# Kernel optimization log

Measured on AMD Instinct MI355X. Metric: run time of the kernel, lower is better.

The kernel has to match this reference:

```python
import jax, jax.numpy as jnp
import numpy as np

B = 2048        # batch
D_IN = 512      # input_dim
H = 768         # hidden_dim
A = 5001        # num_atoms
RULE_LEN = 4
N_DATA = 56000.0


def setup_inputs() -> dict:
    key = jax.random.key(0)
    ks = jax.random.split(key, 24)
    def w(k, shape, fan):
        return (jax.random.normal(k, shape, jnp.float32) / np.sqrt(fan)).astype(jnp.float32)
    return {
        'x': jax.random.normal(ks[0], (B, D_IN), jnp.float32),
        'x_mask': jax.random.randint(ks[1], (B, A), 0, 2, jnp.int32),
        # linear_base: Linear(512,768) ReLU Linear(768,768) ReLU Linear(768,768)
        'W1': w(ks[2], (H, D_IN), D_IN), 'b1': jnp.zeros((H,), jnp.float32),
        'W2': w(ks[3], (H, H), H),       'b2': jnp.zeros((H,), jnp.float32),
        'W3': w(ks[4], (H, H), H),       'b3': jnp.zeros((H,), jnp.float32),
        # single-layer GRU (input H, hidden H); gates ordered r,z,n as in torch
        'W_ih': w(ks[5], (3 * H, H), H), 'b_ih': jnp.zeros((3 * H,), jnp.float32),
        'W_hh': w(ks[6], (3 * H, H), H), 'b_hh': jnp.zeros((3 * H,), jnp.float32),
        # gru_head: Linear(H, num_atoms)
        'Wh': w(ks[7], (A, H), H), 'bh': jnp.zeros((A,), jnp.float32),
        # atom embedding table
        'ae_weight': jax.random.normal(ks[8], (A, H), jnp.float32) * 0.02,
        # stand-in consequent estimator heads (mu, coverage)
        'w_mu': w(ks[9], (H, 1), H),  'b_mu': jnp.zeros((1,), jnp.float32),
        'w_cov': w(ks[10], (H, 1), H), 'b_cov': jnp.zeros((1,), jnp.float32),
        'alpha': jnp.ones((1,), jnp.float32),
    }


def _gru_step(xt, h, W_ih, b_ih, W_hh, b_hh):
    gi = xt @ W_ih.T + b_ih
    gh = h @ W_hh.T + b_hh
    i_r, i_z, i_n = jnp.split(gi, 3, axis=-1)
    h_r, h_z, h_n = jnp.split(gh, 3, axis=-1)
    r = jax.nn.sigmoid(i_r + h_r)
    z = jax.nn.sigmoid(i_z + h_z)
    n = jnp.tanh(i_n + r * h_n)
    return (1.0 - z) * n + z * h


def reference(x, x_mask, W1, b1, W2, b2, W3, b3, W_ih, b_ih, W_hh, b_hh,
              Wh, bh, ae_weight, w_mu, b_mu, w_cov, b_cov, alpha):
    # base (dnn) encoder -> cls embedding [B, H]
    cls = jax.nn.relu(x @ W1.T + b1)
    cls = jax.nn.relu(cls @ W2.T + b2)
    cls = cls @ W3.T + b3

    ae_det = jax.lax.stop_gradient(ae_weight)  # ae.weight is always detached in the original
    mask = x_mask.astype(jnp.float32)
    h = jnp.zeros_like(cls)
    cur = cls
    probs = []
    idx = None
    gkey = jax.random.key(42)
    batch_idx = jnp.arange(cls.shape[0])

    for j in range(RULE_LEN):
        h = _gru_step(cur, h, W_ih, b_ih, W_hh, b_hh)  # dropout = identity (eval)
        logits = h @ Wh.T + bh  # [B, A]
        if j == 0:
            row_zero = jnp.sum(mask, axis=1) == 0.0
            mask = mask.at[:, 0].set(jnp.where(row_zero, 1.0, mask[:, 0]))
        else:
            mask = jnp.where((idx == 0)[:, None], 0.0, mask)
            mask = mask.at[:, 0].set(1.0)
        masked = jnp.where(mask > 0.0, logits, -jnp.inf)
        # gumbel-softmax, tau=1, hard=True (straight-through)
        u = jax.random.uniform(jax.random.fold_in(gkey, j), masked.shape,
                               jnp.float32, 1e-6, 1.0 - 1e-6)
        g = -jnp.log(-jnp.log(u))
        y_soft = jax.nn.softmax(masked + g, axis=1)
        idx = jnp.argmax(y_soft, axis=1)
        y_hard = jax.nn.one_hot(idx, A, dtype=y_soft.dtype)
        prob = y_hard + y_soft - jax.lax.stop_gradient(y_soft)
        probs.append(prob)
        # scatter zero at the selected atom so it can't repeat
        mask = mask.at[batch_idx, idx].set(0.0)
        cur = cls + prob @ ae_det  # [B, H]

    atom_prob = jnp.stack(probs, axis=1)  # [B, rule_len, A]
    atoms = jnp.einsum('bra,ad->brd', atom_prob, ae_det)  # [B, rule_len, H]

    # stand-in consequent estimator: (mu, coverage) from summed atoms
    a = jnp.sum(atoms, axis=1)
    mu = jax.nn.sigmoid(a @ w_mu + b_mu)[:, 0]
    coverage = jax.nn.sigmoid(a @ w_cov + b_cov)[:, 0]

    n = coverage * N_DATA
    inv = alpha[0] / n
    pp = (mu + inv) / (1.0 + 2.0 * inv)
    cp = jnp.stack([1.0 - pp, pp], axis=-1)  # [B, 2]
    out = jnp.log(cp)  # head=1 -> mean over heads is identity
    return (out, atom_prob, cp)
```

## Files before the change

### kernel.cpp

```cpp
#include <hip/hip_runtime.h>
#include <stdint.h>
#include <math.h>

#define B_    2048
#define DIN_  512
#define H_    768
#define G3_   2304
#define A_    5001
#define APAD_ 5120
#define RL_   4
#define NDATA_ 56000.0f

typedef _Float16 f16x8 __attribute__((ext_vector_type(8)));
typedef _Float16 f16x4 __attribute__((ext_vector_type(4)));
typedef float    f32x4 __attribute__((ext_vector_type(4)));

__host__ __device__ __forceinline__ void threefry2x32(
    uint32_t k0, uint32_t k1, uint32_t x0, uint32_t x1,
    uint32_t* o0, uint32_t* o1)
{
  const uint32_t ks2 = k0 ^ k1 ^ 0x1BD11BDAu;
#define TF_R(r) { x0 += x1; x1 = (x1 << (r)) | (x1 >> (32 - (r))); x1 ^= x0; }
  x0 += k0; x1 += k1;
  TF_R(13) TF_R(15) TF_R(26) TF_R(6)
  x0 += k1;  x1 += ks2 + 1u;
  TF_R(17) TF_R(29) TF_R(16) TF_R(24)
  x0 += ks2; x1 += k0 + 2u;
  TF_R(13) TF_R(15) TF_R(26) TF_R(6)
  x0 += k0;  x1 += k1 + 3u;
  TF_R(17) TF_R(29) TF_R(16) TF_R(24)
  x0 += k1;  x1 += ks2 + 4u;
  TF_R(13) TF_R(15) TF_R(26) TF_R(6)
  x0 += ks2; x1 += k0 + 5u;
#undef TF_R
  *o0 = x0; *o1 = x1;
}

__device__ __forceinline__ float gumbel_for(uint32_t k0, uint32_t k1, uint32_t n)
{
  uint32_t o0, o1;
  threefry2x32(k0, k1, 0u, n, &o0, &o1);
  const uint32_t bits = o0 ^ o1;
  const float f = __uint_as_float((bits >> 9) | 0x3f800000u);
  const float minv = 1e-6f;
  const float maxv = 1.0f - 1e-6f;
  const float span = maxv - minv;
  float u = __fmul_rn(f, span);
  u = __fadd_rn(u, minv);
  u = __fsub_rn(u, span);
  u = fmaxf(minv, u);
  return -logf(-logf(u));
}

struct HL { _Float16 h, l; };
__device__ __forceinline__ HL split64(float v)
{
  HL r;
  const float s = v * 64.f;
  r.h = (_Float16)s;
  r.l = (_Float16)(s - (float)r.h);
  return r;
}

__device__ __forceinline__ void gload16(const void* g, void* l)
{
  __builtin_amdgcn_global_load_lds(
      (const __attribute__((address_space(1))) void*)g,
      (__attribute__((address_space(3))) void*)l, 16, 0, 0);
}

struct PSJobs {
  const float* src[7];
  _Float16* hi[7];
  _Float16* lo[7];
  int R[7]; int K[7];
  int cum[8];
};

__global__ __launch_bounds__(256)
void presplit_all(PSJobs J)
{
  const int g = blockIdx.x * 256 + threadIdx.x;
  if (g >= J.cum[7]) return;
  int j = 0;
  while (g >= J.cum[j + 1]) ++j;
  const int i = g - J.cum[j];
  const int K = J.K[j];
  const int e = i * 4;
  const int row = e / K;
  float4 f = make_float4(0.f, 0.f, 0.f, 0.f);
  if (row < J.R[j]) f = *(const float4*)(J.src[j] + (size_t)row * K + (e - row * K));
  const HL s0 = split64(f.x), s1 = split64(f.y);
  const HL s2 = split64(f.z), s3 = split64(f.w);
  const f16x4 hv = {s0.h, s1.h, s2.h, s3.h};
  ((f16x4*)J.hi[j])[i] = hv;
  if (J.lo[j]) {
    const f16x4 lv = {s0.l, s1.l, s2.l, s3.l};
    ((f16x4*)J.lo[j])[i] = lv;
  }
}

__global__ __launch_bounds__(256)
void prep_k(const int* __restrict__ xmask, uint8_t* __restrict__ mask,
            const float* __restrict__ Wh, float* __restrict__ wmaxsq,
            const float* __restrict__ x, _Float16* __restrict__ xh,
            _Float16* __restrict__ xl)
{
  const int blk = blockIdx.x, tid = threadIdx.x;
  __shared__ float redf[256];
  __shared__ int   redi[256];
  if (blk < B_) {
    const int b = blk;
    int s = 0;
    for (int a = tid; a < A_; a += 256) {
      const int m = (xmask[(size_t)b * A_ + a] != 0) ? 1 : 0;
      mask[(size_t)b * A_ + a] = (uint8_t)m;
      s += m;
    }
    redi[tid] = s; __syncthreads();
    for (int t = 128; t > 0; t >>= 1) {
      if (tid < t) redi[tid] += redi[tid + t];
      __syncthreads();
    }
    if (tid == 0 && redi[0] == 0) mask[(size_t)b * A_] = 1;
  } else if (blk < B_ + A_) {
    const int a = blk - B_;
    float p = 0.f;
    for (int d = tid; d < H_; d += 256) {
      const float w = Wh[(size_t)a * H_ + d];
      p += w * w;
    }
    redf[tid] = p; __syncthreads();
    for (int t = 128; t > 0; t >>= 1) {
      if (tid < t) redf[tid] += redf[tid + t];
      __syncthreads();
    }
    if (tid == 0) atomicMax((int*)wmaxsq, __float_as_int(redf[0]));
  } else {
    const int i = (blk - B_ - A_) * 256 + tid;
    const int n4 = B_ * DIN_ / 4;
    if (i < n4) {
      const float4 f = ((const float4*)x)[i];
      const HL s0 = split64(f.x), s1 = split64(f.y);
      const HL s2 = split64(f.z), s3 = split64(f.w);
      const f16x4 hv = {s0.h, s1.h, s2.h, s3.h};
      const f16x4 lv = {s0.l, s1.l, s2.l, s3.l};
      ((f16x4*)xh)[i] = hv;
      ((f16x4*)xl)[i] = lv;
    }
  }
}

struct GJob {
  const _Float16 *Ah, *Al, *Bh, *Bl;
  const float* bias;
  float* C;
  _Float16 *Ch, *Cl;
  int M, K, ldc, n0, Nv;
  int npass, act, wsplit, gum;
};
struct GArgs { GJob j[2]; int sx; uint32_t k0, k1; };

__global__ __launch_bounds__(256)
void gemm2job(GArgs P)
{
  __shared__ _Float16 sA[2][128 * 32];
  __shared__ _Float16 sB[2][128 * 32];

  const int jid = (blockIdx.x < P.sx) ? 0 : 1;
  const GJob J = P.j[jid];
  const int bxx = blockIdx.x - (jid ? P.sx : 0);
  const int bm = blockIdx.y * 128;
  if (bm >= J.M) return;
  const int bn = J.n0 + bxx * 128;

  const int tid = threadIdx.x;
  const int lane = tid & 63, wave = tid >> 6;
  const int wx = wave & 1, wy = wave >> 1;
  const int q = lane >> 4, mr = lane & 15;
  const int K = J.K;
  const int np3 = (J.npass == 3);

  f32x4 acc[4][4];
#pragma unroll
  for (int i = 0; i < 4; ++i)
#pragma unroll
    for (int j = 0; j < 4; ++j) acc[i][j] = (f32x4)0.f;

  const int abase = (wy * 64 + mr) * 32 + q * 8;
  const int bbase = (wx * 64 + mr) * 32 + q * 8;

  if (np3) {
    auto stage = [&](int k0) {
#pragma unroll
      for (int t = 0; t < 2; ++t) {
        const int c = wave * 2 + t;
        const int row = c * 16 + (lane >> 2);
        const int kc = (lane & 3) * 8;
        const size_t ga = (size_t)(bm + row) * K + k0 + kc;
        const size_t gb = (size_t)(bn + row) * K + k0 + kc;
        gload16(J.Ah + ga, &sA[0][c * 512]);
        gload16(J.Bh + gb, &sB[0][c * 512]);
        gload16(J.Al + ga, &sA[1][c * 512]);
        gload16(J.Bl + gb, &sB[1][c * 512]);
      }
    };
    stage(0);
    const int T = K / 32;
    for (int t = 0; t < T; ++t) {
      __syncthreads();
      f16x8 ah[4], al[4], bhv[4], blv[4];
#pragma unroll
      for (int mi = 0; mi < 4; ++mi) {
        ah[mi]  = *(const f16x8*)&sA[0][abase + mi * 512];
        bhv[mi] = *(const f16x8*)&sB[0][bbase + mi * 512];
        al[mi]  = *(const f16x8*)&sA[1][abase + mi * 512];
        blv[mi] = *(const f16x8*)&sB[1][bbase + mi * 512];
      }
      __syncthreads();
      if (t + 1 < T) stage((t + 1) * 32);
#pragma unroll
      for (int ni = 0; ni < 4; ++ni)
#pragma unroll
        for (int mi = 0; mi < 4; ++mi) {
          acc[mi][ni] = __builtin_amdgcn_mfma_f32_16x16x32_f16(ah[mi], bhv[ni], acc[mi][ni], 0, 0, 0);
          acc[mi][ni] = __builtin_amdgcn_mfma_f32_16x16x32_f16(al[mi], bhv[ni], acc[mi][ni], 0, 0, 0);
          acc[mi][ni] = __builtin_amdgcn_mfma_f32_16x16x32_f16(ah[mi], blv[ni], acc[mi][ni], 0, 0, 0);
        }
    }
  } else {
    auto stage64 = [&](int k0) {
#pragma unroll
      for (int t = 0; t < 2; ++t) {
        const int c = wave * 2 + t;
        const int row = c * 16 + (lane >> 2);
        const int kc = (lane & 3) * 8;
        const size_t ga = (size_t)(bm + row) * K + k0 + kc;
        const size_t gb = (size_t)(bn + row) * K + k0 + kc;
        gload16(J.Ah + ga, &sA[0][c * 512]);
        gload16(J.Bh + gb, &sB[0][c * 512]);
        gload16(J.Ah + ga + 32, &sA[1][c * 512]);
        gload16(J.Bh + gb + 32, &sB[1][c * 512]);
      }
    };
    stage64(0);
    const int T2 = K / 64;
    for (int t = 0; t < T2; ++t) {
      __syncthreads();
      f16x8 a0[4], b0[4];
#pragma unroll
      for (int mi = 0; mi < 4; ++mi) {
        a0[mi] = *(const f16x8*)&sA[0][abase + mi * 512];
        b0[mi] = *(const f16x8*)&sB[0][bbase + mi * 512];
      }
#pragma unroll
      for (int ni = 0; ni < 4; ++ni)
#pragma unroll
        for (int mi = 0; mi < 4; ++mi)
          acc[mi][ni] = __builtin_amdgcn_mfma_f32_16x16x32_f16(a0[mi], b0[ni], acc[mi][ni], 0, 0, 0);
      f16x8 a1[4], b1[4];
#pragma unroll
      for (int mi = 0; mi < 4; ++mi) {
        a1[mi] = *(const f16x8*)&sA[1][abase + mi * 512];
        b1[mi] = *(const f16x8*)&sB[1][bbase + mi * 512];
      }
      __syncthreads();
      if (t + 1 < T2) stage64((t + 1) * 64);
#pragma unroll
      for (int ni = 0; ni < 4; ++ni)
#pragma unroll
        for (int mi = 0; mi < 4; ++mi)
          acc[mi][ni] = __builtin_amdgcn_mfma_f32_16x16x32_f16(a1[mi], b1[ni], acc[mi][ni], 0, 0, 0);
    }
  }

  const float sc = 1.f / 4096.f;
#pragma unroll
  for (int ni = 0; ni < 4; ++ni) {
    const int n = bn + wx * 64 + ni * 16 + mr;
    if (n >= J.Nv) continue;
    const float bv = J.bias ? J.bias[n] : 0.f;
#pragma unroll
    for (int mi = 0; mi < 4; ++mi) {
      const int m0 = bm + wy * 64 + mi * 16 + q * 4;
#pragma unroll
      for (int r = 0; r < 4; ++r) {
        const int m = m0 + r;
        float v = acc[mi][ni][r] * sc + bv;
        if (J.act) v = fmaxf(v, 0.f);
        if (J.gum) v += gumbel_for(P.k0, P.k1, (uint32_t)(m * J.ldc + n));
        const size_t off = (size_t)m * J.ldc + n;
        if (J.C) J.C[off] = v;
        if (J.wsplit) {
          const HL s = split64(v);
          J.Ch[off] = s.h;
          J.Cl[off] = s.l;
        }
      }
    }
  }
}

__global__ __launch_bounds__(256)
void gru_elem(const float* __restrict__ gi, const float* __restrict__ bhh,
              float* __restrict__ h, _Float16* __restrict__ hh_,
              _Float16* __restrict__ hl_)
{
  const int i = blockIdx.x * 256 + threadIdx.x;
  if (i >= B_ * H_) return;
  const int b = i / H_;
  const int d = i - b * H_;
  const float* gib = gi + (size_t)b * G3_;
  const float ir = gib[d], iz = gib[H_ + d], in_ = gib[2 * H_ + d];
  const float hr = bhh[d], hz = bhh[H_ + d], hn = bhh[2 * H_ + d];
  const float r = 1.f / (1.f + expf(-(ir + hr)));
  const float z = 1.f / (1.f + expf(-(iz + hz)));
  const float n = tanhf(in_ + r * hn);
  const float hv = (1.f - z) * n;
  h[i] = hv;
  const HL s = split64(hv);
  hh_[i] = s.h; hl_[i] = s.l;
}

__global__ __launch_bounds__(256)
void select_step(const float* __restrict__ v, uint8_t* __restrict__ mask,
                 int* __restrict__ idxs, const float* __restrict__ giCls,
                 const float* __restrict__ AeWih, float* __restrict__ atomp,
                 float* __restrict__ hbuf, const float* __restrict__ WhF,
                 const float* __restrict__ bh, const float* __restrict__ wmaxsq,
                 const float* __restrict__ gh, const float* __restrict__ bhh,
                 _Float16* __restrict__ hh_, _Float16* __restrict__ hl_,
                 uint32_t k0, uint32_t k1, int step)
{
  const int b = blockIdx.x, tid = threadIdx.x;
  uint8_t* mrow = mask + (size_t)b * A_;
  __shared__ float vsh[A_];
  __shared__ float hsh[H_];
  __shared__ float gish[G3_];
  __shared__ float sv[256];
  __shared__ int   si[256];
  __shared__ int   s_list[64];
  __shared__ int   s_n;
  __shared__ int   s_sel;

  float hp = 0.f;
  for (int d = tid; d < H_; d += 256) {
    const float t = hbuf[(size_t)b * H_ + d];
    hsh[d] = t; hp += t * t;
  }
  sv[tid] = hp; __syncthreads();
  for (int t = 128; t > 0; t >>= 1) {
    if (tid < t) sv[tid] += sv[tid + t];
    __syncthreads();
  }
  const float hn2 = sv[0];
  __syncthreads();

  if (step > 0) {
    const int prev = idxs[(step - 1) * B_ + b];
    if (prev == 0)
      for (int a = tid; a < A_; a += 256) mrow[a] = 0;
    __syncthreads();
    if (tid == 0) mrow[0] = 1;
  }
  if (tid == 0) s_n = 0;
  __syncthreads();

  const float* vrow = v + (size_t)b * A_;
  float bv = -INFINITY; int bi = A_;
  for (int a = tid; a < A_; a += 256) {
    const float val = mrow[a] ? vrow[a] : -INFINITY;
    vsh[a] = val;
    if (val > bv) { bv = val; bi = a; }
  }
  sv[tid] = bv; si[tid] = bi; __syncthreads();
  for (int t = 128; t > 0; t >>= 1) {
    if (tid < t) {
      const float v2 = sv[tid + t]; const int i2 = si[tid + t];
      if (v2 > sv[tid] || (v2 == sv[tid] && i2 < si[tid])) { sv[tid] = v2; si[tid] = i2; }
    }
    __syncthreads();
  }
  const float amax = sv[0];
  __syncthreads();

  const float delta = 2.0f * 0.0009765625f * sqrtf(hn2 * wmaxsq[0]);
  const float thr = amax - 2.f * delta;

  for (int a = tid; a < A_; a += 256)
    if (vsh[a] >= thr) {
      const int p = atomicAdd(&s_n, 1);
      if (p < 64) s_list[p] = a;
    }
  __syncthreads();
  const int nc = (s_n < 64) ? s_n : 64;

  const uint32_t nbase = (uint32_t)b * (uint32_t)A_;
  float best = -INFINITY; int bestA = A_;
  for (int c = 0; c < nc; ++c) {
    const int a = s_list[c];
    const float* wr = WhF + (size_t)a * H_;
    float p = 0.f;
    for (int d = tid; d < H_; d += 256) p += hsh[d] * wr[d];
    sv[tid] = p; __syncthreads();
    for (int t = 128; t > 0; t >>= 1) {
      if (tid < t) sv[tid] += sv[tid + t];
      __syncthreads();
    }
    if (tid == 0) {
      const float ev = sv[0] + bh[a] + gumbel_for(k0, k1, nbase + (uint32_t)a);
      if (ev > best || (ev == best && a < bestA)) { best = ev; bestA = a; }
    }
    __syncthreads();
  }
  if (tid == 0) {
    s_sel = bestA;
    mrow[bestA] = 0;
    idxs[step * B_ + b] = bestA;
    atomp[(size_t)b * (RL_ * A_) + (size_t)step * A_ + bestA] = 1.0f;
  }
  __syncthreads();

  if (step < RL_ - 1) {
    const int sel = s_sel;
    const float* ar = AeWih + (size_t)sel * G3_;
    const float* gr = giCls + (size_t)b * G3_;
    for (int d = tid; d < G3_; d += 256) gish[d] = gr[d] + ar[d];
    __syncthreads();
    const float* ghb = gh + (size_t)b * G3_;
    for (int d = tid; d < H_; d += 256) {
      const float r = 1.f / (1.f + expf(-(gish[d] + ghb[d])));
      const float z = 1.f / (1.f + expf(-(gish[H_ + d] + ghb[H_ + d])));
      const float n = tanhf(gish[2 * H_ + d] + r * ghb[2 * H_ + d]);
      const float hv = (1.f - z) * n + z * hsh[d];
      hbuf[(size_t)b * H_ + d] = hv;
      const HL s = split64(hv);
      hh_[(size_t)b * H_ + d] = s.h;
      hl_[(size_t)b * H_ + d] = s.l;
    }
  }
}

__global__ __launch_bounds__(256)
void head_k(const int* __restrict__ idxs, const float* __restrict__ ae,
            const float* __restrict__ w_mu, const float* __restrict__ b_mu,
            const float* __restrict__ w_cov, const float* __restrict__ b_cov,
            const float* __restrict__ alpha, float* __restrict__ outf)
{
  const int b = blockIdx.x, tid = threadIdx.x;
  const int i0 = idxs[0 * B_ + b], i1 = idxs[1 * B_ + b];
  const int i2 = idxs[2 * B_ + b], i3 = idxs[3 * B_ + b];
  const float* r0 = ae + (size_t)i0 * H_;
  const float* r1 = ae + (size_t)i1 * H_;
  const float* r2 = ae + (size_t)i2 * H_;
  const float* r3 = ae + (size_t)i3 * H_;
  float pmu = 0.f, pcv = 0.f;
  for (int d = tid; d < H_; d += 256) {
    const float a = r0[d] + r1[d] + r2[d] + r3[d];
    pmu += a * w_mu[d];
    pcv += a * w_cov[d];
  }
  __shared__ float smu[256], scv[256];
  smu[tid] = pmu; scv[tid] = pcv;
  __syncthreads();
  for (int s = 128; s > 0; s >>= 1) {
    if (tid < s) { smu[tid] += smu[tid + s]; scv[tid] += scv[tid + s]; }
    __syncthreads();
  }
  if (tid == 0) {
    const float mu = 1.f / (1.f + expf(-(smu[0] + b_mu[0])));
    const float cv = 1.f / (1.f + expf(-(scv[0] + b_cov[0])));
    const float n = cv * NDATA_;
    const float inv = alpha[0] / n;
    const float pp = (mu + inv) / (1.f + 2.f * inv);
    outf[2 * b + 0] = logf(1.f - pp);
    outf[2 * b + 1] = logf(pp);
    float* cp = outf + 2 * B_ + (size_t)B_ * RL_ * A_;
    cp[2 * b + 0] = 1.f - pp;
    cp[2 * b + 1] = pp;
  }
}

extern "C" void kernel_launch(void* const* d_in, const int* in_sizes, int n_in,
                              void* d_out, int out_size, void* d_ws, size_t ws_size,
                              hipStream_t stream)
{
  const float* x     = (const float*)d_in[0];
  const int*   xmask = (const int*)d_in[1];
  const float* W1 = (const float*)d_in[2];  const float* b1 = (const float*)d_in[3];
  const float* W2 = (const float*)d_in[4];  const float* b2 = (const float*)d_in[5];
  const float* W3 = (const float*)d_in[6];  const float* b3 = (const float*)d_in[7];
  const float* Wih = (const float*)d_in[8]; const float* bih = (const float*)d_in[9];
  const float* Whh = (const float*)d_in[10];const float* bhh = (const float*)d_in[11];
  const float* Wh = (const float*)d_in[12]; const float* bh = (const float*)d_in[13];
  const float* ae = (const float*)d_in[14];
  const float* w_mu = (const float*)d_in[15];  const float* b_mu = (const float*)d_in[16];
  const float* w_cov = (const float*)d_in[17]; const float* b_cov = (const float*)d_in[18];
  const float* alpha = (const float*)d_in[19];

  char* ws = (char*)d_ws;
  size_t off = 0;
  auto alloc = [&](size_t bytes) -> void* {
    void* p = ws + off;
    off += (bytes + 255) & ~(size_t)255;
    return p;
  };
  float* hbuf   = (float*)alloc((size_t)B_ * H_ * 4);
  float* giCls  = (float*)alloc((size_t)B_ * G3_ * 4);
  float* gh     = (float*)alloc((size_t)B_ * G3_ * 4);
  float* vbuf   = (float*)alloc((size_t)B_ * A_ * 4);
  float* AeWih  = (float*)alloc((size_t)APAD_ * G3_ * 4);
  uint8_t* mask = (uint8_t*)alloc((size_t)B_ * A_);
  int* idxs     = (int*)alloc((size_t)RL_ * B_ * 4);
  _Float16* hh_ = (_Float16*)alloc((size_t)B_ * H_ * 2);
  _Float16* hl_ = (_Float16*)alloc((size_t)B_ * H_ * 2);
  _Float16* clsh = (_Float16*)alloc((size_t)B_ * H_ * 2);
  _Float16* clsl = (_Float16*)alloc((size_t)B_ * H_ * 2);
  _Float16* xh  = (_Float16*)alloc((size_t)B_ * DIN_ * 2);
  _Float16* xl  = (_Float16*)alloc((size_t)B_ * DIN_ * 2);
  _Float16* t1h = (_Float16*)alloc((size_t)B_ * H_ * 2);
  _Float16* t1l = (_Float16*)alloc((size_t)B_ * H_ * 2);
  _Float16* t2h = (_Float16*)alloc((size_t)B_ * H_ * 2);
  _Float16* t2l = (_Float16*)alloc((size_t)B_ * H_ * 2);
  _Float16* w1h = (_Float16*)alloc((size_t)H_ * DIN_ * 2);
  _Float16* w1l = (_Float16*)alloc((size_t)H_ * DIN_ * 2);
  _Float16* w2h = (_Float16*)alloc((size_t)H_ * H_ * 2);
  _Float16* w2l = (_Float16*)alloc((size_t)H_ * H_ * 2);
  _Float16* w3h = (_Float16*)alloc((size_t)H_ * H_ * 2);
  _Float16* w3l = (_Float16*)alloc((size_t)H_ * H_ * 2);
  _Float16* wihh = (_Float16*)alloc((size_t)G3_ * H_ * 2);
  _Float16* wihl = (_Float16*)alloc((size_t)G3_ * H_ * 2);
  _Float16* whhh = (_Float16*)alloc((size_t)G3_ * H_ * 2);
  _Float16* whhl = (_Float16*)alloc((size_t)G3_ * H_ * 2);
  _Float16* whhi = (_Float16*)alloc((size_t)APAD_ * H_ * 2);
  _Float16* aeh  = (_Float16*)alloc((size_t)APAD_ * H_ * 2);
  _Float16* ael  = (_Float16*)alloc((size_t)APAD_ * H_ * 2);
  float* wmaxsq = (float*)alloc(4);

  float* outf  = (float*)d_out;
  float* atomp = outf + 2 * B_;

  (void)hipMemsetAsync(d_out, 0, (size_t)out_size * sizeof(float), stream);
  (void)hipMemsetAsync(wmaxsq, 0, 4, stream);

  PSJobs J;
  const float* srcs[7] = {W1, W2, W3, Wih, Whh, Wh, ae};
  _Float16* his[7] = {w1h, w2h, w3h, wihh, whhh, whhi, aeh};
  _Float16* los[7] = {w1l, w2l, w3l, wihl, whhl, nullptr, ael};
  const int Rs[7]    = {H_, H_, H_, G3_, G3_, A_, A_};
  const int Rpads[7] = {H_, H_, H_, G3_, G3_, APAD_, APAD_};
  const int Ks[7]    = {DIN_, H_, H_, H_, H_, H_, H_};
  J.cum[0] = 0;
  for (int j = 0; j < 7; ++j) {
    J.src[j] = srcs[j]; J.hi[j] = his[j]; J.lo[j] = los[j];
    J.R[j] = Rs[j]; J.K[j] = Ks[j];
    J.cum[j + 1] = J.cum[j] + Rpads[j] * Ks[j] / 4;
  }
  presplit_all<<<(J.cum[7] + 255) / 256, 256, 0, stream>>>(J);

  prep_k<<<B_ + A_ + (B_ * DIN_ / 4 + 255) / 256, 256, 0, stream>>>(
      xmask, mask, Wh, wmaxsq, x, xh, xl);

  auto mkjob = [](const _Float16* Ah, const _Float16* Al, const _Float16* Bh,
                  const _Float16* Bl, const float* bias, float* C,
                  _Float16* Ch, _Float16* Cl, int M, int K, int ldc,
                  int n0, int Nv, int npass, int act, int wsplit, int gum) {
    GJob g; g.Ah = Ah; g.Al = Al; g.Bh = Bh; g.Bl = Bl; g.bias = bias;
    g.C = C; g.Ch = Ch; g.Cl = Cl; g.M = M; g.K = K; g.ldc = ldc;
    g.n0 = n0; g.Nv = Nv; g.npass = npass; g.act = act; g.wsplit = wsplit;
    g.gum = gum;
    return g;
  };
  auto aejob = [&](int t0) {
    return mkjob(aeh, ael, wihh, wihl, nullptr, AeWih, nullptr, nullptr,
                 APAD_, H_, G3_, t0 * 128, G3_, 3, 0, 0, 0);
  };

  {
    GArgs P;
    P.j[0] = mkjob(xh, xl, w1h, w1l, b1, nullptr, t1h, t1l,
                   B_, DIN_, H_, 0, H_, 3, 1, 1, 0);
    P.j[1] = aejob(0);
    P.sx = H_ / 128; P.k0 = 0; P.k1 = 0;
    gemm2job<<<dim3(H_ / 128 + 5, APAD_ / 128), 256, 0, stream>>>(P);
  }
  {
    GArgs P;
    P.j[0] = mkjob(t1h, t1l, w2h, w2l, b2, nullptr, t2h, t2l,
                   B_, H_, H_, 0, H_, 3, 1, 1, 0);
    P.j[1] = aejob(5);
    P.sx = H_ / 128; P.k0 = 0; P.k1 = 0;
    gemm2job<<<dim3(H_ / 128 + 5, APAD_ / 128), 256, 0, stream>>>(P);
  }
  {
    GArgs P;
    P.j[0] = mkjob(t2h, t2l, w3h, w3l, b3, nullptr, clsh, clsl,
                   B_, H_, H_, 0, H_, 3, 0, 1, 0);
    P.j[1] = aejob(10);
    P.sx = H_ / 128; P.k0 = 0; P.k1 = 0;
    gemm2job<<<dim3(H_ / 128 + 4, APAD_ / 128), 256, 0, stream>>>(P);
  }
  {
    GArgs P;
    P.j[0] = mkjob(clsh, clsl, wihh, wihl, bih, giCls, nullptr, nullptr,
                   B_, H_, G3_, 0, G3_, 3, 0, 0, 0);
    P.j[1] = aejob(14);
    P.sx = G3_ / 128; P.k0 = 0; P.k1 = 0;
    gemm2job<<<dim3(G3_ / 128 + 4, APAD_ / 128), 256, 0, stream>>>(P);
  }

  uint32_t fk0[RL_], fk1[RL_];
  for (int j = 0; j < RL_; ++j)
    threefry2x32(0u, 42u, 0u, (uint32_t)j, &fk0[j], &fk1[j]);

  gru_elem<<<(B_ * H_ + 255) / 256, 256, 0, stream>>>(giCls, bhh, hbuf, hh_, hl_);

  for (int j = 0; j < RL_; ++j) {
    GArgs P;
    P.j[0] = mkjob(hh_, nullptr, whhi, nullptr, bh, vbuf, nullptr, nullptr,
                   B_, H_, A_, 0, A_, 1, 0, 0, 1);
    const int gx0 = APAD_ / 128;
    int gx = gx0;
    if (j < RL_ - 1) {
      P.j[1] = mkjob(hh_, hl_, whhh, whhl, bhh, gh, nullptr, nullptr,
                     B_, H_, G3_, 0, G3_, 3, 0, 0, 0);
      gx += G3_ / 128;
    } else {
      P.j[1] = P.j[0];
    }
    P.sx = gx0; P.k0 = fk0[j]; P.k1 = fk1[j];
    gemm2job<<<dim3(gx, B_ / 128), 256, 0, stream>>>(P);

    select_step<<<B_, 256, 0, stream>>>(vbuf, mask, idxs, giCls, AeWih, atomp,
                                        hbuf, Wh, bh, wmaxsq, gh, bhh, hh_, hl_,
                                        fk0[j], fk1[j], j);
  }

  head_k<<<B_, 256, 0, stream>>>(idxs, ae, w_mu, b_mu, w_cov, b_cov, alpha, outf);
}
```

Before: 1.043 ms.

## Fold W3 into W_ih to drop a GEMM stage and trim select_step shared memory

```diff
diff --git a/kernel.cpp b/kernel.cpp
--- a/kernel.cpp
+++ b/kernel.cpp
@@ -73,7 +73,7 @@
   const float* src[7];
   _Float16* hi[7];
   _Float16* lo[7];
-  int R[7]; int K[7];
+  int R[7]; int K[7]; int trans[7];
   int cum[8];
 };
 
@@ -88,8 +88,17 @@
   const int K = J.K[j];
   const int e = i * 4;
   const int row = e / K;
+  const int col = e - row * K;
   float4 f = make_float4(0.f, 0.f, 0.f, 0.f);
-  if (row < J.R[j]) f = *(const float4*)(J.src[j] + (size_t)row * K + (e - row * K));
+  if (J.trans[j]) {
+    const int R = J.R[j];
+    f.x = J.src[j][(size_t)(col + 0) * R + row];
+    f.y = J.src[j][(size_t)(col + 1) * R + row];
+    f.z = J.src[j][(size_t)(col + 2) * R + row];
+    f.w = J.src[j][(size_t)(col + 3) * R + row];
+  } else if (row < J.R[j]) {
+    f = *(const float4*)(J.src[j] + (size_t)row * K + col);
+  }
   const HL s0 = split64(f.x), s1 = split64(f.y);
   const HL s2 = split64(f.z), s3 = split64(f.w);
   const f16x4 hv = {s0.h, s1.h, s2.h, s3.h};
@@ -104,9 +113,12 @@
 void prep_k(const int* __restrict__ xmask, uint8_t* __restrict__ mask,
             const float* __restrict__ Wh, float* __restrict__ wmaxsq,
             const float* __restrict__ x, _Float16* __restrict__ xh,
-            _Float16* __restrict__ xl)
+            _Float16* __restrict__ xl, const float* __restrict__ Wih,
+            const float* __restrict__ b3, const float* __restrict__ bih,
+            float* __restrict__ bprime)
 {
   const int blk = blockIdx.x, tid = threadIdx.x;
+  const int XB = (B_ * DIN_ / 4 + 255) / 256;
   __shared__ float redf[256];
   __shared__ int   redi[256];
   if (blk < B_) {
@@ -136,7 +148,7 @@
       __syncthreads();
     }
     if (tid == 0) atomicMax((int*)wmaxsq, __float_as_int(redf[0]));
-  } else {
+  } else if (blk < B_ + A_ + XB) {
     const int i = (blk - B_ - A_) * 256 + tid;
     const int n4 = B_ * DIN_ / 4;
     if (i < n4) {
@@ -148,6 +160,17 @@
       ((f16x4*)xh)[i] = hv;
       ((f16x4*)xl)[i] = lv;
     }
+  } else {
+    const int n = blk - B_ - A_ - XB;
+    float p = 0.f;
+    for (int d = tid; d < H_; d += 256)
+      p += Wih[(size_t)n * H_ + d] * b3[d];
+    redf[tid] = p; __syncthreads();
+    for (int t = 128; t > 0; t >>= 1) {
+      if (tid < t) redf[tid] += redf[tid + t];
+      __syncthreads();
+    }
+    if (tid == 0) bprime[n] = redf[0] + bih[n];
   }
 }
 
@@ -159,7 +182,7 @@
   int M, K, ldc, n0, Nv;
   int npass, act, wsplit, gum;
 };
-struct GArgs { GJob j[2]; int sx; uint32_t k0, k1; };
+struct GArgs { GJob j[3]; int sx1, sx2; uint32_t k0, k1; };
 
 __global__ __launch_bounds__(256)
 void gemm2job(GArgs P)
@@ -167,9 +190,10 @@
   __shared__ _Float16 sA[2][128 * 32];
   __shared__ _Float16 sB[2][128 * 32];
 
-  const int jid = (blockIdx.x < P.sx) ? 0 : 1;
+  const int bx = blockIdx.x;
+  const int jid = (bx < P.sx1) ? 0 : ((bx < P.sx2) ? 1 : 2);
   const GJob J = P.j[jid];
-  const int bxx = blockIdx.x - (jid ? P.sx : 0);
+  const int bxx = bx - ((jid == 0) ? 0 : ((jid == 1) ? P.sx1 : P.sx2));
   const int bm = blockIdx.y * 128;
   if (bm >= J.M) return;
   const int bn = J.n0 + bxx * 128;
@@ -334,9 +358,7 @@
 {
   const int b = blockIdx.x, tid = threadIdx.x;
   uint8_t* mrow = mask + (size_t)b * A_;
-  __shared__ float vsh[A_];
   __shared__ float hsh[H_];
-  __shared__ float gish[G3_];
   __shared__ float sv[256];
   __shared__ int   si[256];
   __shared__ int   s_list[64];
@@ -370,7 +392,6 @@
   float bv = -INFINITY; int bi = A_;
   for (int a = tid; a < A_; a += 256) {
     const float val = mrow[a] ? vrow[a] : -INFINITY;
-    vsh[a] = val;
     if (val > bv) { bv = val; bi = a; }
   }
   sv[tid] = bv; si[tid] = bi; __syncthreads();
@@ -388,7 +409,7 @@
   const float thr = amax - 2.f * delta;
 
   for (int a = tid; a < A_; a += 256)
-    if (vsh[a] >= thr) {
+    if (mrow[a] && vrow[a] >= thr) {
       const int p = atomicAdd(&s_n, 1);
       if (p < 64) s_list[p] = a;
     }
@@ -425,13 +446,14 @@
     const int sel = s_sel;
     const float* ar = AeWih + (size_t)sel * G3_;
     const float* gr = giCls + (size_t)b * G3_;
-    for (int d = tid; d < G3_; d += 256) gish[d] = gr[d] + ar[d];
-    __syncthreads();
     const float* ghb = gh + (size_t)b * G3_;
     for (int d = tid; d < H_; d += 256) {
-      const float r = 1.f / (1.f + expf(-(gish[d] + ghb[d])));
-      const float z = 1.f / (1.f + expf(-(gish[H_ + d] + ghb[H_ + d])));
-      const float n = tanhf(gish[2 * H_ + d] + r * ghb[2 * H_ + d]);
+      const float g0 = gr[d] + ar[d];
+      const float g1 = gr[H_ + d] + ar[H_ + d];
+      const float g2 = gr[2 * H_ + d] + ar[2 * H_ + d];
+      const float r = 1.f / (1.f + expf(-(g0 + ghb[d])));
+      const float z = 1.f / (1.f + expf(-(g1 + ghb[H_ + d])));
+      const float n = tanhf(g2 + r * ghb[2 * H_ + d]);
       const float hv = (1.f - z) * n + z * hsh[d];
       hbuf[(size_t)b * H_ + d] = hv;
       const HL s = split64(hv);
@@ -514,8 +536,6 @@
   int* idxs     = (int*)alloc((size_t)RL_ * B_ * 4);
   _Float16* hh_ = (_Float16*)alloc((size_t)B_ * H_ * 2);
   _Float16* hl_ = (_Float16*)alloc((size_t)B_ * H_ * 2);
-  _Float16* clsh = (_Float16*)alloc((size_t)B_ * H_ * 2);
-  _Float16* clsl = (_Float16*)alloc((size_t)B_ * H_ * 2);
   _Float16* xh  = (_Float16*)alloc((size_t)B_ * DIN_ * 2);
   _Float16* xl  = (_Float16*)alloc((size_t)B_ * DIN_ * 2);
   _Float16* t1h = (_Float16*)alloc((size_t)B_ * H_ * 2);
@@ -526,8 +546,8 @@
   _Float16* w1l = (_Float16*)alloc((size_t)H_ * DIN_ * 2);
   _Float16* w2h = (_Float16*)alloc((size_t)H_ * H_ * 2);
   _Float16* w2l = (_Float16*)alloc((size_t)H_ * H_ * 2);
-  _Float16* w3h = (_Float16*)alloc((size_t)H_ * H_ * 2);
-  _Float16* w3l = (_Float16*)alloc((size_t)H_ * H_ * 2);
+  _Float16* w3th = (_Float16*)alloc((size_t)H_ * H_ * 2);
+  _Float16* w3tl = (_Float16*)alloc((size_t)H_ * H_ * 2);
   _Float16* wihh = (_Float16*)alloc((size_t)G3_ * H_ * 2);
   _Float16* wihl = (_Float16*)alloc((size_t)G3_ * H_ * 2);
   _Float16* whhh = (_Float16*)alloc((size_t)G3_ * H_ * 2);
@@ -535,6 +555,9 @@
   _Float16* whhi = (_Float16*)alloc((size_t)APAD_ * H_ * 2);
   _Float16* aeh  = (_Float16*)alloc((size_t)APAD_ * H_ * 2);
   _Float16* ael  = (_Float16*)alloc((size_t)APAD_ * H_ * 2);
+  _Float16* wph  = (_Float16*)alloc((size_t)G3_ * H_ * 2);
+  _Float16* wpl  = (_Float16*)alloc((size_t)G3_ * H_ * 2);
+  float* bprime = (float*)alloc((size_t)G3_ * 4);
   float* wmaxsq = (float*)alloc(4);
 
   float* outf  = (float*)d_out;
@@ -545,21 +568,23 @@
 
   PSJobs J;
   const float* srcs[7] = {W1, W2, W3, Wih, Whh, Wh, ae};
-  _Float16* his[7] = {w1h, w2h, w3h, wihh, whhh, whhi, aeh};
-  _Float16* los[7] = {w1l, w2l, w3l, wihl, whhl, nullptr, ael};
+  _Float16* his[7] = {w1h, w2h, w3th, wihh, whhh, whhi, aeh};
+  _Float16* los[7] = {w1l, w2l, w3tl, wihl, whhl, nullptr, ael};
   const int Rs[7]    = {H_, H_, H_, G3_, G3_, A_, A_};
   const int Rpads[7] = {H_, H_, H_, G3_, G3_, APAD_, APAD_};
   const int Ks[7]    = {DIN_, H_, H_, H_, H_, H_, H_};
+  const int Trs[7]   = {0, 0, 1, 0, 0, 0, 0};
   J.cum[0] = 0;
   for (int j = 0; j < 7; ++j) {
     J.src[j] = srcs[j]; J.hi[j] = his[j]; J.lo[j] = los[j];
-    J.R[j] = Rs[j]; J.K[j] = Ks[j];
+    J.R[j] = Rs[j]; J.K[j] = Ks[j]; J.trans[j] = Trs[j];
     J.cum[j + 1] = J.cum[j] + Rpads[j] * Ks[j] / 4;
   }
   presplit_all<<<(J.cum[7] + 255) / 256, 256, 0, stream>>>(J);
 
-  prep_k<<<B_ + A_ + (B_ * DIN_ / 4 + 255) / 256, 256, 0, stream>>>(
-      xmask, mask, Wh, wmaxsq, x, xh, xl);
+  const int XB = (B_ * DIN_ / 4 + 255) / 256;
+  prep_k<<<B_ + A_ + XB + G3_, 256, 0, stream>>>(
+      xmask, mask, Wh, wmaxsq, x, xh, xl, Wih, b3, bih, bprime);
 
   auto mkjob = [](const _Float16* Ah, const _Float16* Al, const _Float16* Bh,
                   const _Float16* Bl, const float* bias, float* C,
@@ -580,33 +605,29 @@
     GArgs P;
     P.j[0] = mkjob(xh, xl, w1h, w1l, b1, nullptr, t1h, t1l,
                    B_, DIN_, H_, 0, H_, 3, 1, 1, 0);
-    P.j[1] = aejob(0);
-    P.sx = H_ / 128; P.k0 = 0; P.k1 = 0;
-    gemm2job<<<dim3(H_ / 128 + 5, APAD_ / 128), 256, 0, stream>>>(P);
+    P.j[1] = mkjob(wihh, wihl, w3th, w3tl, nullptr, nullptr, wph, wpl,
+                   G3_, H_, H_, 0, H_, 3, 0, 1, 0);
+    P.j[2] = aejob(0);
+    P.sx1 = H_ / 128; P.sx2 = H_ / 128 + H_ / 128; P.k0 = 0; P.k1 = 0;
+    gemm2job<<<dim3(P.sx2 + 6, APAD_ / 128), 256, 0, stream>>>(P);
   }
   {
     GArgs P;
     P.j[0] = mkjob(t1h, t1l, w2h, w2l, b2, nullptr, t2h, t2l,
                    B_, H_, H_, 0, H_, 3, 1, 1, 0);
-    P.j[1] = aejob(5);
-    P.sx = H_ / 128; P.k0 = 0; P.k1 = 0;
-    gemm2job<<<dim3(H_ / 128 + 5, APAD_ / 128), 256, 0, stream>>>(P);
+    P.j[1] = aejob(6);
+    P.j[2] = P.j[1];
+    P.sx1 = H_ / 128; P.sx2 = H_ / 128 + 6; P.k0 = 0; P.k1 = 0;
+    gemm2job<<<dim3(P.sx2, APAD_ / 128), 256, 0, stream>>>(P);
   }
   {
     GArgs P;
-    P.j[0] = mkjob(t2h, t2l, w3h, w3l, b3, nullptr, clsh, clsl,
-                   B_, H_, H_, 0, H_, 3, 0, 1, 0);
-    P.j[1] = aejob(10);
-    P.sx = H_ / 128; P.k0 = 0; P.k1 = 0;
-    gemm2job<<<dim3(H_ / 128 + 4, APAD_ / 128), 256, 0, stream>>>(P);
-  }
-  {
-    GArgs P;
-    P.j[0] = mkjob(clsh, clsl, wihh, wihl, bih, giCls, nullptr, nullptr,
+    P.j[0] = mkjob(t2h, t2l, wph, wpl, bprime, giCls, nullptr, nullptr,
                    B_, H_, G3_, 0, G3_, 3, 0, 0, 0);
-    P.j[1] = aejob(14);
-    P.sx = G3_ / 128; P.k0 = 0; P.k1 = 0;
-    gemm2job<<<dim3(G3_ / 128 + 4, APAD_ / 128), 256, 0, stream>>>(P);
+    P.j[1] = aejob(12);
+    P.j[2] = P.j[1];
+    P.sx1 = G3_ / 128; P.sx2 = G3_ / 128 + 6; P.k0 = 0; P.k1 = 0;
+    gemm2job<<<dim3(P.sx2, APAD_ / 128), 256, 0, stream>>>(P);
   }
 
   uint32_t fk0[RL_], fk1[RL_];
@@ -628,7 +649,8 @@
     } else {
       P.j[1] = P.j[0];
     }
-    P.sx = gx0; P.k0 = fk0[j]; P.k1 = fk1[j];
+    P.j[2] = P.j[1];
+    P.sx1 = gx0; P.sx2 = gx; P.k0 = fk0[j]; P.k1 = fk1[j];
     gemm2job<<<dim3(gx, B_ / 128), 256, 0, stream>>>(P);
 
     select_step<<<B_, 256, 0, stream>>>(vbuf, mask, idxs, giCls, AeWih, atomp,
```

Result: faster. 981.3 us (-5.9%).
